# Kernel optimization log

Hardware: AMD Instinct MI355X
Metric: run time of the kernel (lower is better)

The kernel has to match this reference:

```python
import jax, jax.numpy as jnp
import numpy as np

B, C, H, W = 8, 64, 128, 128
C8 = C // 8  # query/key channels


def setup_inputs() -> dict:
    key = jax.random.key(0)
    ks = jax.random.split(key, 9)
    s = 0.05
    return {
        "x": jax.random.normal(ks[0], (B, C, H, W), jnp.float32),
        "y": jax.random.normal(ks[1], (B, C, H, W), jnp.float32),
        "Wq": jax.random.normal(ks[2], (C8, C), jnp.float32) * s,
        "bq": jax.random.normal(ks[3], (C8,), jnp.float32) * s,
        "Wk": jax.random.normal(ks[4], (C8, C), jnp.float32) * s,
        "bk": jax.random.normal(ks[5], (C8,), jnp.float32) * s,
        "Wv": jax.random.normal(ks[6], (C, 2 * C), jnp.float32) * s,
        "bv": jax.random.normal(ks[7], (C,), jnp.float32) * s,
        "gamma": jnp.float32(0.5),
    }


def reference(x, y, Wq, bq, Wk, bk, Wv, bv, gamma):
    b, c, h, w = x.shape
    # 1x1 convs as channel contractions
    q = jnp.einsum('bchw,oc->bohw', x, Wq) + bq[None, :, None, None]   # [B,C8,H,W]
    k = jnp.einsum('bchw,oc->bohw', y, Wk) + bk[None, :, None, None]   # [B,C8,H,W]
    v = jnp.einsum('bchw,oc->bohw', jnp.concatenate([x, y], axis=1), Wv) \
        + bv[None, :, None, None]                                      # [B,C,H,W]

    # column (height) attention energies: e[b,i,w,j] = sum_c q[b,c,i,w] k[b,c,j,w]
    eH = jnp.einsum('bciw,bcjw->biwj', q, k)                           # [B,H,W,H]
    diag = jnp.eye(h, dtype=bool)[:, None, :]                          # [H,1,H] (i==j)
    eH = jnp.where(diag[None], -jnp.inf, eH)
    # row (width) attention energies: e[b,h,i,j] = sum_c q[b,c,h,i] k[b,c,h,j]
    eW = jnp.einsum('bchi,bchj->bhij', q, k)                           # [B,H,W,W]

    # fused softmax over concatenated H+W attention targets
    att = jax.nn.softmax(jnp.concatenate([eH, eW], axis=3), axis=3)    # [B,H,W,H+W]
    aH, aW = att[..., :h], att[..., h:]

    outH = jnp.einsum('bcjw,biwj->bciw', v, aH)                        # [B,C,H,W]
    outW = jnp.einsum('bchj,bhij->bchi', v, aW)                        # [B,C,H,W]
    return gamma * (outH + outW) + x + y
```

## Files before the change

kernel.cpp:

```cpp
#include <hip/hip_runtime.h>
#include <hip/hip_bf16.h>

#define BDIM 8
#define CDIM 64
#define C8DIM 8
#define HDIM 128
#define WDIM 128
#define HW (HDIM * WDIM)

typedef short bf16x8 __attribute__((ext_vector_type(8)));
typedef float f32x4 __attribute__((ext_vector_type(4)));

__device__ inline unsigned pk_bf16(float a, float b) {
    unsigned ua = (unsigned)__bfloat16_as_ushort(__float2bfloat16(a));
    unsigned ub = (unsigned)__bfloat16_as_ushort(__float2bfloat16(b));
    return ua | (ub << 16);
}
__device__ inline void cvt2(unsigned u, float& lo, float& hi) {
    lo = __uint_as_float(u << 16);
    hi = __uint_as_float(u & 0xffff0000u);
}

__global__ __launch_bounds__(256) void qkv_kernel(
    const float* __restrict__ x, const float* __restrict__ y,
    const float* __restrict__ Wq, const float* __restrict__ bq,
    const float* __restrict__ Wk, const float* __restrict__ bk,
    const float* __restrict__ Wv, const float* __restrict__ bv,
    uint4* __restrict__ q_pm, uint4* __restrict__ k_pm, uint4* __restrict__ v_pm,
    uint4* __restrict__ xy_pm)
{
    __shared__ ushort smem[128 * 88];
    __shared__ float  sb[80];

    const int t = threadIdx.x;

    for (int i = t; i < 80 * 64; i += 256) {
        int o  = i >> 6;
        int cp = i & 63;
        int c  = cp * 2;
        float w0, w1;
        if (o < 8) {
            if (c < 64) { w0 = Wq[o * 64 + c]; w1 = Wq[o * 64 + c + 1]; }
            else        { w0 = 0.f; w1 = 0.f; }
        } else if (o < 16) {
            if (c >= 64) { w0 = Wk[(o - 8) * 64 + c - 64]; w1 = Wk[(o - 8) * 64 + c - 63]; }
            else         { w0 = 0.f; w1 = 0.f; }
        } else {
            w0 = Wv[(o - 16) * 128 + c];
            w1 = Wv[(o - 16) * 128 + c + 1];
        }
        ((unsigned*)smem)[o * 64 + (cp ^ ((o & 7) << 2))] = pk_bf16(w0, w1);
    }
    if (t < 80) {
        sb[t] = (t < 8) ? bq[t] : (t < 16) ? bk[t - 8] : bv[t - 16];
    }
    __syncthreads();

    const int blk = blockIdx.x;
    const int b   = blk & 7;
    const int p0  = (blk >> 3) << 7;

    const int wv = t >> 6, ln = t & 63, lg = ln >> 4, li = ln & 15;
    const int pcol0 = p0 + wv * 32 + li;

    const float* xb = x + (size_t)b * CDIM * HW;
    const float* yb = y + (size_t)b * CDIM * HW;

    f32x4 acc[5][2];
    #pragma unroll
    for (int mt = 0; mt < 5; mt++)
        #pragma unroll
        for (int n = 0; n < 2; n++) acc[mt][n] = (f32x4){0.f, 0.f, 0.f, 0.f};

    uint4 xys[2][2];

    #pragma unroll
    for (int pair = 0; pair < 2; pair++) {
        const int chb = pair * 32 + lg * 8;
        const float* xp = xb + (size_t)chb * HW;
        const float* yp = yb + (size_t)chb * HW;
        bf16x8 bx[2], by[2];
        #pragma unroll
        for (int n = 0; n < 2; n++) {
            const size_t poff = (size_t)(pcol0 + n * 16);
            float fx[8], fy[8];
            #pragma unroll
            for (int e = 0; e < 8; e++) {
                fx[e] = xp[(size_t)e * HW + poff];
                fy[e] = yp[(size_t)e * HW + poff];
            }
            uint4 ux, uy, s;
            ux.x = pk_bf16(fx[0], fx[1]); ux.y = pk_bf16(fx[2], fx[3]);
            ux.z = pk_bf16(fx[4], fx[5]); ux.w = pk_bf16(fx[6], fx[7]);
            uy.x = pk_bf16(fy[0], fy[1]); uy.y = pk_bf16(fy[2], fy[3]);
            uy.z = pk_bf16(fy[4], fy[5]); uy.w = pk_bf16(fy[6], fy[7]);
            s.x = pk_bf16(fx[0] + fy[0], fx[1] + fy[1]);
            s.y = pk_bf16(fx[2] + fy[2], fx[3] + fy[3]);
            s.z = pk_bf16(fx[4] + fy[4], fx[5] + fy[5]);
            s.w = pk_bf16(fx[6] + fy[6], fx[7] + fy[7]);
            bx[n] = *(bf16x8*)&ux;
            by[n] = *(bf16x8*)&uy;
            xys[pair][n] = s;
        }
        #pragma unroll
        for (int mt = 0; mt < 5; mt++) {
            const int row = mt * 16 + li;
            const int sw  = ((li & 7) << 3);
            bf16x8 ax = *(const bf16x8*)&smem[row * 128 + ((pair * 32 + lg * 8) ^ sw)];
            bf16x8 ay = *(const bf16x8*)&smem[row * 128 + (((2 + pair) * 32 + lg * 8) ^ sw)];
            #pragma unroll
            for (int n = 0; n < 2; n++) {
                acc[mt][n] = __builtin_amdgcn_mfma_f32_16x16x32_bf16(ax, bx[n], acc[mt][n], 0, 0, 0);
                acc[mt][n] = __builtin_amdgcn_mfma_f32_16x16x32_bf16(ay, by[n], acc[mt][n], 0, 0, 0);
            }
        }
    }
    __syncthreads();

    #pragma unroll
    for (int mt = 0; mt < 5; mt++) {
        const int ob = mt * 16 + lg * 4;
        const float b0 = sb[ob + 0], b1 = sb[ob + 1], b2 = sb[ob + 2], b3 = sb[ob + 3];
        #pragma unroll
        for (int n = 0; n < 2; n++) {
            const int pl = wv * 32 + n * 16 + li;
            uint2 w;
            w.x = pk_bf16(acc[mt][n][0] + b0, acc[mt][n][1] + b1);
            w.y = pk_bf16(acc[mt][n][2] + b2, acc[mt][n][3] + b3);
            *(uint2*)&smem[pl * 88 + ob] = w;
        }
    }
    __syncthreads();

    const size_t gpb = (size_t)b * HW + p0;
    if (t < 128) {
        q_pm[gpb + t] = *(const uint4*)&smem[t * 88 + 0];
    } else {
        k_pm[gpb + (t - 128)] = *(const uint4*)&smem[(t - 128) * 88 + 8];
    }
    #pragma unroll
    for (int i2 = 0; i2 < 4; i2++) {
        const int f = t + i2 * 256;
        const int p = f >> 3, q8 = f & 7;
        v_pm[(gpb + p) * 8 + q8] = *(const uint4*)&smem[p * 88 + 16 + q8 * 8];
    }

    if (xy_pm) {
        __syncthreads();
        #pragma unroll
        for (int pair = 0; pair < 2; pair++)
            #pragma unroll
            for (int n = 0; n < 2; n++) {
                const int pl = wv * 32 + n * 16 + li;
                *(uint4*)&smem[pl * 72 + pair * 32 + lg * 8] = xys[pair][n];
            }
        __syncthreads();
        #pragma unroll
        for (int i2 = 0; i2 < 4; i2++) {
            const int f = t + i2 * 256;
            const int p = f >> 3, q8 = f & 7;
            xy_pm[(gpb + p) * 8 + q8] = *(const uint4*)&smem[p * 72 + q8 * 8];
        }
    }
}

__global__ __launch_bounds__(256, 2) void colattn_kernel(
    const uint4* __restrict__ q_pm, const uint4* __restrict__ k_pm,
    const uint4* __restrict__ v_pm,
    ushort* __restrict__ H_t, float* __restrict__ mH_g, float* __restrict__ sH_g)
{
    __shared__ ushort Q_lds[128 * 8];
    __shared__ ushort K_lds[128 * 8];
    __shared__ ushort V_lds[64 * 136];
    __shared__ ushort P_lds[128 * 136];

    const int blk = blockIdx.x;
    const int b  = blk & 7;
    const int cc = blk >> 3;
    const int t  = threadIdx.x;

    if (t < 128) {
        *(uint4*)&Q_lds[t * 8] = q_pm[(size_t)b * HW + (size_t)t * 128 + cc];
    } else {
        int j = t - 128;
        *(uint4*)&K_lds[j * 8] = k_pm[(size_t)b * HW + (size_t)j * 128 + cc];
    }
    {
        int j = t & 127, h = t >> 7;
        const uint4* vp = v_pm + ((size_t)b * HW + (size_t)j * 128 + cc) * 8 + 4 * h;
        #pragma unroll
        for (int qd = 0; qd < 4; qd++) {
            uint4 vu = vp[qd];
            int ch0 = 32 * h + 8 * qd;
            V_lds[(ch0 + 0) * 136 + j] = (ushort)(vu.x & 0xffff);
            V_lds[(ch0 + 1) * 136 + j] = (ushort)(vu.x >> 16);
            V_lds[(ch0 + 2) * 136 + j] = (ushort)(vu.y & 0xffff);
            V_lds[(ch0 + 3) * 136 + j] = (ushort)(vu.y >> 16);
            V_lds[(ch0 + 4) * 136 + j] = (ushort)(vu.z & 0xffff);
            V_lds[(ch0 + 5) * 136 + j] = (ushort)(vu.z >> 16);
            V_lds[(ch0 + 6) * 136 + j] = (ushort)(vu.w & 0xffff);
            V_lds[(ch0 + 7) * 136 + j] = (ushort)(vu.w >> 16);
        }
    }
    __syncthreads();

    const int wv = t >> 6, ln = t & 63, lg = ln >> 4, li = ln & 15;
    const bf16x8 zf = {0, 0, 0, 0, 0, 0, 0, 0};

    bf16x8 afr[8], bfr[2];
    #pragma unroll
    for (int jt = 0; jt < 8; jt++)
        afr[jt] = (lg == 0) ? *(const bf16x8*)&K_lds[(jt * 16 + li) * 8] : zf;
    #pragma unroll
    for (int it2 = 0; it2 < 2; it2++)
        bfr[it2] = (lg == 0) ? *(const bf16x8*)&Q_lds[((2 * wv + it2) * 16 + li) * 8] : zf;

    f32x4 dfr[2][8];
    #pragma unroll
    for (int a = 0; a < 2; a++)
        #pragma unroll
        for (int jt = 0; jt < 8; jt++) dfr[a][jt] = (f32x4){0.f, 0.f, 0.f, 0.f};

    #pragma unroll
    for (int it2 = 0; it2 < 2; it2++)
        #pragma unroll
        for (int jt = 0; jt < 8; jt++)
            dfr[it2][jt] = __builtin_amdgcn_mfma_f32_16x16x32_bf16(
                afr[jt], bfr[it2], dfr[it2][jt], 0, 0, 0);

    #pragma unroll
    for (int it2 = 0; it2 < 2; it2++) {
        const int i = (2 * wv + it2) * 16 + li;
        float m = -1e30f;
        #pragma unroll
        for (int jt = 0; jt < 8; jt++)
            #pragma unroll
            for (int rr = 0; rr < 4; rr++) {
                int j = jt * 16 + lg * 4 + rr;
                float e = dfr[it2][jt][rr];
                if (j == i) e = -1e30f;
                dfr[it2][jt][rr] = e;
                m = fmaxf(m, e);
            }
        m = fmaxf(m, __shfl_xor(m, 16));
        m = fmaxf(m, __shfl_xor(m, 32));
        float s = 0.f;
        #pragma unroll
        for (int jt = 0; jt < 8; jt++)
            #pragma unroll
            for (int rr = 0; rr < 4; rr++) {
                float p = __expf(dfr[it2][jt][rr] - m);
                dfr[it2][jt][rr] = p;
                s += p;
            }
        s += __shfl_xor(s, 16);
        s += __shfl_xor(s, 32);
        #pragma unroll
        for (int jt = 0; jt < 8; jt++) {
            uint2 w;
            w.x = pk_bf16(dfr[it2][jt][0], dfr[it2][jt][1]);
            w.y = pk_bf16(dfr[it2][jt][2], dfr[it2][jt][3]);
            *(uint2*)&P_lds[(size_t)i * 136 + jt * 16 + lg * 4] = w;
        }
        if (lg == 0) {
            mH_g[((size_t)b * 128 + cc) * 128 + i] = m;
            sH_g[((size_t)b * 128 + cc) * 128 + i] = s;
        }
    }
    __syncthreads();

    f32x4 ofr[8];
    #pragma unroll
    for (int itl = 0; itl < 8; itl++) ofr[itl] = (f32x4){0.f, 0.f, 0.f, 0.f};

    #pragma unroll
    for (int ks = 0; ks < 4; ks++) {
        const int jb = ks * 32 + lg * 8;
        bf16x8 av = *(const bf16x8*)&V_lds[(wv * 16 + li) * 136 + jb];
        #pragma unroll
        for (int itl = 0; itl < 8; itl++) {
            bf16x8 bp = *(const bf16x8*)&P_lds[(itl * 16 + li) * 136 + jb];
            ofr[itl] = __builtin_amdgcn_mfma_f32_16x16x32_bf16(av, bp, ofr[itl], 0, 0, 0);
        }
    }

    #pragma unroll
    for (int itl = 0; itl < 8; itl++) {
        const int i = itl * 16 + li;
        uint2 w;
        w.x = pk_bf16(ofr[itl][0], ofr[itl][1]);
        w.y = pk_bf16(ofr[itl][2], ofr[itl][3]);
        *(uint2*)&H_t[(((size_t)b * 128 + i) * 128 + cc) * 64 + wv * 16 + lg * 4] = w;
    }
}

template<int USE_XY>
__global__ __launch_bounds__(256, 2) void rowattn_kernel(
    const uint4* __restrict__ q_pm, const uint4* __restrict__ k_pm,
    const uint4* __restrict__ v_pm,
    const ushort* __restrict__ H_t, const float* __restrict__ mH_g,
    const float* __restrict__ sH_g,
    const float* __restrict__ x, const float* __restrict__ y,
    const ushort* __restrict__ xy_pm,
    const float* __restrict__ gptr, float* __restrict__ out)
{
    __shared__ ushort Q_lds[128 * 8];
    __shared__ ushort K_lds[128 * 8];
    __shared__ ushort V_lds[64 * 136];
    __shared__ ushort P_lds[128 * 136];
    __shared__ float mW_s[128], sW_s[128];

    const int blk = blockIdx.x;
    const int b = blk & 7;
    const int r = blk >> 3;
    const int t = threadIdx.x;

    if (t < 128) {
        *(uint4*)&Q_lds[t * 8] = q_pm[(size_t)b * HW + (size_t)r * 128 + t];
    } else {
        int j = t - 128;
        *(uint4*)&K_lds[j * 8] = k_pm[(size_t)b * HW + (size_t)r * 128 + j];
    }
    {
        int j = t & 127, h = t >> 7;
        const uint4* vp = v_pm + ((size_t)b * HW + (size_t)r * 128 + j) * 8 + 4 * h;
        #pragma unroll
        for (int qd = 0; qd < 4; qd++) {
            uint4 vu = vp[qd];
            int ch0 = 32 * h + 8 * qd;
            V_lds[(ch0 + 0) * 136 + j] = (ushort)(vu.x & 0xffff);
            V_lds[(ch0 + 1) * 136 + j] = (ushort)(vu.x >> 16);
            V_lds[(ch0 + 2) * 136 + j] = (ushort)(vu.y & 0xffff);
            V_lds[(ch0 + 3) * 136 + j] = (ushort)(vu.y >> 16);
            V_lds[(ch0 + 4) * 136 + j] = (ushort)(vu.z & 0xffff);
            V_lds[(ch0 + 5) * 136 + j] = (ushort)(vu.z >> 16);
            V_lds[(ch0 + 6) * 136 + j] = (ushort)(vu.w & 0xffff);
            V_lds[(ch0 + 7) * 136 + j] = (ushort)(vu.w >> 16);
        }
    }
    __syncthreads();

    const int wv = t >> 6, ln = t & 63, lg = ln >> 4, li = ln & 15;
    const bf16x8 zf = {0, 0, 0, 0, 0, 0, 0, 0};

    bf16x8 afr[8], bfr[2];
    #pragma unroll
    for (int jt = 0; jt < 8; jt++)
        afr[jt] = (lg == 0) ? *(const bf16x8*)&K_lds[(jt * 16 + li) * 8] : zf;
    #pragma unroll
    for (int it2 = 0; it2 < 2; it2++)
        bfr[it2] = (lg == 0) ? *(const bf16x8*)&Q_lds[((2 * wv + it2) * 16 + li) * 8] : zf;

    f32x4 dfr[2][8];
    #pragma unroll
    for (int a = 0; a < 2; a++)
        #pragma unroll
        for (int jt = 0; jt < 8; jt++) dfr[a][jt] = (f32x4){0.f, 0.f, 0.f, 0.f};

    #pragma unroll
    for (int it2 = 0; it2 < 2; it2++)
        #pragma unroll
        for (int jt = 0; jt < 8; jt++)
            dfr[it2][jt] = __builtin_amdgcn_mfma_f32_16x16x32_bf16(
                afr[jt], bfr[it2], dfr[it2][jt], 0, 0, 0);

    #pragma unroll
    for (int it2 = 0; it2 < 2; it2++) {
        const int i = (2 * wv + it2) * 16 + li;
        float m = -1e30f;
        #pragma unroll
        for (int jt = 0; jt < 8; jt++)
            #pragma unroll
            for (int rr = 0; rr < 4; rr++)
                m = fmaxf(m, dfr[it2][jt][rr]);
        m = fmaxf(m, __shfl_xor(m, 16));
        m = fmaxf(m, __shfl_xor(m, 32));
        float s = 0.f;
        #pragma unroll
        for (int jt = 0; jt < 8; jt++)
            #pragma unroll
            for (int rr = 0; rr < 4; rr++) {
                float p = __expf(dfr[it2][jt][rr] - m);
                dfr[it2][jt][rr] = p;
                s += p;
            }
        s += __shfl_xor(s, 16);
        s += __shfl_xor(s, 32);
        #pragma unroll
        for (int jt = 0; jt < 8; jt++) {
            uint2 w;
            w.x = pk_bf16(dfr[it2][jt][0], dfr[it2][jt][1]);
            w.y = pk_bf16(dfr[it2][jt][2], dfr[it2][jt][3]);
            *(uint2*)&P_lds[(size_t)i * 136 + jt * 16 + lg * 4] = w;
        }
        if (lg == 0) {
            mW_s[i] = m;
            sW_s[i] = s;
        }
    }
    __syncthreads();

    f32x4 ofr[8];
    #pragma unroll
    for (int itl = 0; itl < 8; itl++) ofr[itl] = (f32x4){0.f, 0.f, 0.f, 0.f};

    #pragma unroll
    for (int ks = 0; ks < 4; ks++) {
        const int jb = ks * 32 + lg * 8;
        bf16x8 av = *(const bf16x8*)&V_lds[(wv * 16 + li) * 136 + jb];
        #pragma unroll
        for (int itl = 0; itl < 8; itl++) {
            bf16x8 bp = *(const bf16x8*)&P_lds[(itl * 16 + li) * 136 + jb];
            ofr[itl] = __builtin_amdgcn_mfma_f32_16x16x32_bf16(av, bp, ofr[itl], 0, 0, 0);
        }
    }

    const float gamma = gptr[0];
    #pragma unroll
    for (int itl = 0; itl < 8; itl++) {
        const int i = itl * 16 + li;
        float mWv = mW_s[i], sWv = sW_s[i];
        float mHv = mH_g[((size_t)b * 128 + i) * 128 + r];
        float sHv = sH_g[((size_t)b * 128 + i) * 128 + r];
        float m  = fmaxf(mHv, mWv);
        float wH = __expf(mHv - m);
        float wW = __expf(mWv - m);
        float invg = gamma / (sHv * wH + sWv * wW);

        uint2 hw = *(const uint2*)&H_t[(((size_t)b * 128 + r) * 128 + i) * 64 + wv * 16 + lg * 4];
        float h[4];
        cvt2(hw.x, h[0], h[1]);
        cvt2(hw.y, h[2], h[3]);

        float resid[4];
        if (USE_XY) {
            uint2 xu = *(const uint2*)&xy_pm[((size_t)b * HW + (size_t)r * 128 + i) * 64 + wv * 16 + lg * 4];
            cvt2(xu.x, resid[0], resid[1]);
            cvt2(xu.y, resid[2], resid[3]);
        }

        #pragma unroll
        for (int rr = 0; rr < 4; rr++) {
            const int ch = wv * 16 + lg * 4 + rr;
            size_t o = (((size_t)b * 64 + ch) * 128 + r) * 128 + i;
            float res = USE_XY ? resid[rr] : (x[o] + y[o]);
            out[o] = (h[rr] * wH + ofr[itl][rr] * wW) * invg + res;
        }
    }
}

extern "C" void kernel_launch(void* const* d_in, const int* in_sizes, int n_in,
                              void* d_out, int out_size, void* d_ws, size_t ws_size,
                              hipStream_t stream)
{
    const float* x     = (const float*)d_in[0];
    const float* y     = (const float*)d_in[1];
    const float* Wq    = (const float*)d_in[2];
    const float* bq    = (const float*)d_in[3];
    const float* Wk    = (const float*)d_in[4];
    const float* bk    = (const float*)d_in[5];
    const float* Wv    = (const float*)d_in[6];
    const float* bv    = (const float*)d_in[7];
    const float* gamma = (const float*)d_in[8];
    float* out = (float*)d_out;

    uint4*  q_pm = (uint4*)d_ws;
    uint4*  k_pm = q_pm + (size_t)BDIM * HW;
    uint4*  v_pm = k_pm + (size_t)BDIM * HW;
    ushort* H_t  = (ushort*)(v_pm + (size_t)BDIM * HW * 8);
    float*  mH   = (float*)(H_t + (size_t)BDIM * HW * 64);
    float*  sH   = mH + (size_t)BDIM * HW;
    ushort* xy   = (ushort*)(sH + (size_t)BDIM * HW);
    size_t need  = (size_t)((char*)(xy + (size_t)BDIM * HW * 64) - (char*)d_ws);
    const bool use_xy = ws_size >= need;

    qkv_kernel<<<dim3(BDIM * HW / 128), dim3(256), 0, stream>>>(
        x, y, Wq, bq, Wk, bk, Wv, bv, q_pm, k_pm, v_pm,
        use_xy ? (uint4*)xy : (uint4*)nullptr);

    colattn_kernel<<<dim3(BDIM * WDIM), dim3(256), 0, stream>>>(
        q_pm, k_pm, v_pm, H_t, mH, sH);

    if (use_xy) {
        rowattn_kernel<1><<<dim3(BDIM * HDIM), dim3(256), 0, stream>>>(
            q_pm, k_pm, v_pm, H_t, mH, sH, x, y, xy, gamma, out);
    } else {
        rowattn_kernel<0><<<dim3(BDIM * HDIM), dim3(256), 0, stream>>>(
            q_pm, k_pm, v_pm, H_t, mH, sH, x, y, xy, gamma, out);
    }
}
```

Before: 73.38 us.

## Process two pixel tiles per QKV block and stage column-attention output through LDS

The QKV projection kernel now handles two 128-pixel tiles per block with half the grid. The weight matrix is loaded into shared memory once and reused for both tiles, and the second tile's global loads are issued before the first tile's results are stored, so load latency overlaps with the epilogue. Separately, the column-attention kernel writes its output into LDS first and then stores to H_t as 16-byte coalesced vectors instead of scattered 8-byte writes. The cost is more registers for double-buffered tiles, a larger LDS footprint in qkv, and two extra barriers in colattn.

Result: faster. 66.56 us (-9.3%).

```diff
diff --git a/kernel.cpp b/kernel.cpp
--- a/kernel.cpp
+++ b/kernel.cpp
@@ -29,7 +29,8 @@
     uint4* __restrict__ q_pm, uint4* __restrict__ k_pm, uint4* __restrict__ v_pm,
     uint4* __restrict__ xy_pm)
 {
-    __shared__ ushort smem[128 * 88];
+    __shared__ ushort sW[80 * 128];
+    __shared__ ushort sOut[128 * 88];
     __shared__ float  sb[80];
 
     const int t = threadIdx.x;
@@ -49,7 +50,7 @@
             w0 = Wv[(o - 16) * 128 + c];
             w1 = Wv[(o - 16) * 128 + c + 1];
         }
-        ((unsigned*)smem)[o * 64 + (cp ^ ((o & 7) << 2))] = pk_bf16(w0, w1);
+        ((unsigned*)sW)[o * 64 + (cp ^ ((o & 7) << 2))] = pk_bf16(w0, w1);
     }
     if (t < 80) {
         sb[t] = (t < 8) ? bq[t] : (t < 16) ? bk[t - 8] : bv[t - 16];
@@ -58,110 +59,135 @@
 
     const int blk = blockIdx.x;
     const int b   = blk & 7;
-    const int p0  = (blk >> 3) << 7;
+    const int p0A = ((blk >> 3) * 2) << 7;
+    const int p0B = p0A + 128;
 
     const int wv = t >> 6, ln = t & 63, lg = ln >> 4, li = ln & 15;
-    const int pcol0 = p0 + wv * 32 + li;
 
     const float* xb = x + (size_t)b * CDIM * HW;
     const float* yb = y + (size_t)b * CDIM * HW;
 
-    f32x4 acc[5][2];
-    #pragma unroll
-    for (int mt = 0; mt < 5; mt++)
-        #pragma unroll
-        for (int n = 0; n < 2; n++) acc[mt][n] = (f32x4){0.f, 0.f, 0.f, 0.f};
-
-    uint4 xys[2][2];
-
-    #pragma unroll
-    for (int pair = 0; pair < 2; pair++) {
-        const int chb = pair * 32 + lg * 8;
-        const float* xp = xb + (size_t)chb * HW;
-        const float* yp = yb + (size_t)chb * HW;
-        bf16x8 bx[2], by[2];
-        #pragma unroll
-        for (int n = 0; n < 2; n++) {
-            const size_t poff = (size_t)(pcol0 + n * 16);
-            float fx[8], fy[8];
-            #pragma unroll
-            for (int e = 0; e < 8; e++) {
-                fx[e] = xp[(size_t)e * HW + poff];
-                fy[e] = yp[(size_t)e * HW + poff];
-            }
-            uint4 ux, uy, s;
-            ux.x = pk_bf16(fx[0], fx[1]); ux.y = pk_bf16(fx[2], fx[3]);
-            ux.z = pk_bf16(fx[4], fx[5]); ux.w = pk_bf16(fx[6], fx[7]);
-            uy.x = pk_bf16(fy[0], fy[1]); uy.y = pk_bf16(fy[2], fy[3]);
-            uy.z = pk_bf16(fy[4], fy[5]); uy.w = pk_bf16(fy[6], fy[7]);
-            s.x = pk_bf16(fx[0] + fy[0], fx[1] + fy[1]);
-            s.y = pk_bf16(fx[2] + fy[2], fx[3] + fy[3]);
-            s.z = pk_bf16(fx[4] + fy[4], fx[5] + fy[5]);
-            s.w = pk_bf16(fx[6] + fy[6], fx[7] + fy[7]);
-            bx[n] = *(bf16x8*)&ux;
-            by[n] = *(bf16x8*)&uy;
-            xys[pair][n] = s;
-        }
+    auto load_tile = [&](int p0, bf16x8 (&bx)[2][2], bf16x8 (&by)[2][2],
+                         uint4 (&xys)[2][2]) {
+        #pragma unroll
+        for (int pair = 0; pair < 2; pair++) {
+            const int chb = pair * 32 + lg * 8;
+            const float* xp = xb + (size_t)chb * HW;
+            const float* yp = yb + (size_t)chb * HW;
+            #pragma unroll
+            for (int n = 0; n < 2; n++) {
+                const size_t poff = (size_t)(p0 + wv * 32 + n * 16 + li);
+                float fx[8], fy[8];
+                #pragma unroll
+                for (int e = 0; e < 8; e++) {
+                    fx[e] = xp[(size_t)e * HW + poff];
+                    fy[e] = yp[(size_t)e * HW + poff];
+                }
+                uint4 ux, uy, s;
+                ux.x = pk_bf16(fx[0], fx[1]); ux.y = pk_bf16(fx[2], fx[3]);
+                ux.z = pk_bf16(fx[4], fx[5]); ux.w = pk_bf16(fx[6], fx[7]);
+                uy.x = pk_bf16(fy[0], fy[1]); uy.y = pk_bf16(fy[2], fy[3]);
+                uy.z = pk_bf16(fy[4], fy[5]); uy.w = pk_bf16(fy[6], fy[7]);
+                s.x = pk_bf16(fx[0] + fy[0], fx[1] + fy[1]);
+                s.y = pk_bf16(fx[2] + fy[2], fx[3] + fy[3]);
+                s.z = pk_bf16(fx[4] + fy[4], fx[5] + fy[5]);
+                s.w = pk_bf16(fx[6] + fy[6], fx[7] + fy[7]);
+                bx[pair][n] = *(bf16x8*)&ux;
+                by[pair][n] = *(bf16x8*)&uy;
+                xys[pair][n] = s;
+            }
+        }
+    };
+
+    auto gemm_tile = [&](const bf16x8 (&bx)[2][2], const bf16x8 (&by)[2][2],
+                         f32x4 (&acc)[5][2]) {
+        #pragma unroll
+        for (int pair = 0; pair < 2; pair++) {
+            #pragma unroll
+            for (int mt = 0; mt < 5; mt++) {
+                const int row = mt * 16 + li;
+                const int sw  = ((li & 7) << 3);
+                bf16x8 ax = *(const bf16x8*)&sW[row * 128 + ((pair * 32 + lg * 8) ^ sw)];
+                bf16x8 ay = *(const bf16x8*)&sW[row * 128 + (((2 + pair) * 32 + lg * 8) ^ sw)];
+                #pragma unroll
+                for (int n = 0; n < 2; n++) {
+                    acc[mt][n] = __builtin_amdgcn_mfma_f32_16x16x32_bf16(ax, bx[pair][n], acc[mt][n], 0, 0, 0);
+                    acc[mt][n] = __builtin_amdgcn_mfma_f32_16x16x32_bf16(ay, by[pair][n], acc[mt][n], 0, 0, 0);
+                }
+            }
+        }
+    };
+
+    auto store_tile = [&](int p0, const f32x4 (&acc)[5][2], const uint4 (&xys)[2][2]) {
+        __syncthreads();
         #pragma unroll
         for (int mt = 0; mt < 5; mt++) {
-            const int row = mt * 16 + li;
-            const int sw  = ((li & 7) << 3);
-            bf16x8 ax = *(const bf16x8*)&smem[row * 128 + ((pair * 32 + lg * 8) ^ sw)];
-            bf16x8 ay = *(const bf16x8*)&smem[row * 128 + (((2 + pair) * 32 + lg * 8) ^ sw)];
-            #pragma unroll
-            for (int n = 0; n < 2; n++) {
-                acc[mt][n] = __builtin_amdgcn_mfma_f32_16x16x32_bf16(ax, bx[n], acc[mt][n], 0, 0, 0);
-                acc[mt][n] = __builtin_amdgcn_mfma_f32_16x16x32_bf16(ay, by[n], acc[mt][n], 0, 0, 0);
-            }
-        }
-    }
-    __syncthreads();
-
-    #pragma unroll
-    for (int mt = 0; mt < 5; mt++) {
-        const int ob = mt * 16 + lg * 4;
-        const float b0 = sb[ob + 0], b1 = sb[ob + 1], b2 = sb[ob + 2], b3 = sb[ob + 3];
-        #pragma unroll
-        for (int n = 0; n < 2; n++) {
-            const int pl = wv * 32 + n * 16 + li;
-            uint2 w;
-            w.x = pk_bf16(acc[mt][n][0] + b0, acc[mt][n][1] + b1);
-            w.y = pk_bf16(acc[mt][n][2] + b2, acc[mt][n][3] + b3);
-            *(uint2*)&smem[pl * 88 + ob] = w;
-        }
-    }
-    __syncthreads();
-
-    const size_t gpb = (size_t)b * HW + p0;
-    if (t < 128) {
-        q_pm[gpb + t] = *(const uint4*)&smem[t * 88 + 0];
-    } else {
-        k_pm[gpb + (t - 128)] = *(const uint4*)&smem[(t - 128) * 88 + 8];
-    }
-    #pragma unroll
-    for (int i2 = 0; i2 < 4; i2++) {
-        const int f = t + i2 * 256;
-        const int p = f >> 3, q8 = f & 7;
-        v_pm[(gpb + p) * 8 + q8] = *(const uint4*)&smem[p * 88 + 16 + q8 * 8];
-    }
-
-    if (xy_pm) {
-        __syncthreads();
-        #pragma unroll
-        for (int pair = 0; pair < 2; pair++)
+            const int ob = mt * 16 + lg * 4;
+            const float b0 = sb[ob + 0], b1 = sb[ob + 1], b2 = sb[ob + 2], b3 = sb[ob + 3];
             #pragma unroll
             for (int n = 0; n < 2; n++) {
                 const int pl = wv * 32 + n * 16 + li;
-                *(uint4*)&smem[pl * 72 + pair * 32 + lg * 8] = xys[pair][n];
-            }
+                uint2 w;
+                w.x = pk_bf16(acc[mt][n][0] + b0, acc[mt][n][1] + b1);
+                w.y = pk_bf16(acc[mt][n][2] + b2, acc[mt][n][3] + b3);
+                *(uint2*)&sOut[pl * 88 + ob] = w;
+            }
+        }
         __syncthreads();
+        const size_t gpb = (size_t)b * HW + p0;
+        if (t < 128) {
+            q_pm[gpb + t] = *(const uint4*)&sOut[t * 88 + 0];
+        } else {
+            k_pm[gpb + (t - 128)] = *(const uint4*)&sOut[(t - 128) * 88 + 8];
+        }
         #pragma unroll
         for (int i2 = 0; i2 < 4; i2++) {
             const int f = t + i2 * 256;
             const int p = f >> 3, q8 = f & 7;
-            xy_pm[(gpb + p) * 8 + q8] = *(const uint4*)&smem[p * 72 + q8 * 8];
-        }
-    }
+            v_pm[(gpb + p) * 8 + q8] = *(const uint4*)&sOut[p * 88 + 16 + q8 * 8];
+        }
+        if (xy_pm) {
+            __syncthreads();
+            #pragma unroll
+            for (int pair = 0; pair < 2; pair++)
+                #pragma unroll
+                for (int n = 0; n < 2; n++) {
+                    const int pl = wv * 32 + n * 16 + li;
+                    *(uint4*)&sOut[pl * 72 + pair * 32 + lg * 8] = xys[pair][n];
+                }
+            __syncthreads();
+            #pragma unroll
+            for (int i2 = 0; i2 < 4; i2++) {
+                const int f = t + i2 * 256;
+                const int p = f >> 3, q8 = f & 7;
+                xy_pm[(gpb + p) * 8 + q8] = *(const uint4*)&sOut[p * 72 + q8 * 8];
+            }
+        }
+    };
+
+    bf16x8 bxA[2][2], byA[2][2], bxB[2][2], byB[2][2];
+    uint4  xyA[2][2], xyB[2][2];
+    f32x4  acc[5][2];
+
+    load_tile(p0A, bxA, byA, xyA);
+
+    #pragma unroll
+    for (int mt = 0; mt < 5; mt++)
+        #pragma unroll
+        for (int n = 0; n < 2; n++) acc[mt][n] = (f32x4){0.f, 0.f, 0.f, 0.f};
+    gemm_tile(bxA, byA, acc);
+
+    load_tile(p0B, bxB, byB, xyB);
+
+    store_tile(p0A, acc, xyA);
+
+    #pragma unroll
+    for (int mt = 0; mt < 5; mt++)
+        #pragma unroll
+        for (int n = 0; n < 2; n++) acc[mt][n] = (f32x4){0.f, 0.f, 0.f, 0.f};
+    gemm_tile(bxB, byB, acc);
+
+    store_tile(p0B, acc, xyB);
 }
 
 __global__ __launch_bounds__(256, 2) void colattn_kernel(
@@ -283,6 +309,7 @@
             ofr[itl] = __builtin_amdgcn_mfma_f32_16x16x32_bf16(av, bp, ofr[itl], 0, 0, 0);
         }
     }
+    __syncthreads();
 
     #pragma unroll
     for (int itl = 0; itl < 8; itl++) {
@@ -290,7 +317,16 @@
         uint2 w;
         w.x = pk_bf16(ofr[itl][0], ofr[itl][1]);
         w.y = pk_bf16(ofr[itl][2], ofr[itl][3]);
-        *(uint2*)&H_t[(((size_t)b * 128 + i) * 128 + cc) * 64 + wv * 16 + lg * 4] = w;
+        *(uint2*)&P_lds[i * 72 + wv * 16 + lg * 4] = w;
+    }
+    __syncthreads();
+
+    #pragma unroll
+    for (int i2 = 0; i2 < 4; i2++) {
+        const int f = t + i2 * 256;
+        const int i = f >> 3, cb = (f & 7) * 8;
+        *(uint4*)&H_t[(((size_t)b * 128 + i) * 128 + cc) * 64 + cb] =
+            *(const uint4*)&P_lds[i * 72 + cb];
     }
 }
 
@@ -474,7 +510,7 @@
     size_t need  = (size_t)((char*)(xy + (size_t)BDIM * HW * 64) - (char*)d_ws);
     const bool use_xy = ws_size >= need;
 
-    qkv_kernel<<<dim3(BDIM * HW / 128), dim3(256), 0, stream>>>(
+    qkv_kernel<<<dim3(BDIM * HW / 256), dim3(256), 0, stream>>>(
         x, y, Wq, bq, Wk, bk, Wv, bv, q_pm, k_pm, v_pm,
         use_xy ? (uint4*)xy : (uint4*)nullptr);
 
```
